# Optimization experiments

Hardware: AMD Instinct MI355X
Metric: run time of the kernel (lower is better)

## Reference

```python
import jax, jax.numpy as jnp
import numpy as np

FS = 4096.0
TRAIN_KERNEL = 4
TRAIN_STRIDE = 0.25
BATCH = 1024
NPERSEG = 4096          # fftlength * fs
NOVERLAP = NPERSEG // 2 # default overlap
FL, FH = 20.0, 500.0


def _welch(data):
    """Faithful port of _torch_welch with average='mean' (which is a SUM over segments
    in the original code), off by the same constant factor as the original."""
    N, nsample = data.shape
    nstride = NPERSEG - NOVERLAP
    nseg = int(np.ceil((nsample - NPERSEG) / nstride)) + 1
    # frame indices [nseg, nperseg] (static numpy -> cheap gather)
    idx = np.arange(nseg)[:, None] * nstride + np.arange(NPERSEG)[None, :]
    frames = data[:, idx]                                   # [N, nseg, nperseg]
    n = np.arange(NPERSEG)
    window = (0.5 - 0.5 * np.cos(2.0 * np.pi * n / NPERSEG)).astype(np.float32) * 2.0  # periodic hann * 2
    fd = jnp.fft.rfft(frames * window, axis=-1)             # [N, nseg, nfreq]
    power = jnp.real(fd) ** 2 + jnp.imag(fd) ** 2
    psd = jnp.sum(power, axis=1)                            # original 'mean' branch uses sum
    T = nsample * FS
    return psd / T                                          # [N, nfreq]


def setup_inputs() -> dict:
    key = jax.random.key(0)
    k1, k2 = jax.random.split(key)
    T = int(TRAIN_KERNEL * FS)  # 16384
    pred = jax.random.normal(k1, (BATCH, T), dtype=jnp.float32)
    target = jax.random.normal(k2, (BATCH, T), dtype=jnp.float32)
    return {"pred": pred, "target": target}


def reference(pred, target):
    res = target - pred
    s = int(TRAIN_STRIDE * FS)                     # 1024 samples per stride
    shape_x = int(TRAIN_KERNEL / TRAIN_STRIDE)     # 16
    # cross[i] = res[:, i*s:(i+1)*s].flatten() -> reshape/transpose, no loop
    def to_cross(x):
        return x[:, : shape_x * s].reshape(BATCH, shape_x, s).transpose(1, 0, 2).reshape(shape_x, BATCH * s)
    cross_res = to_cross(res)
    cross_target = to_cross(target)

    psd_res = _welch(cross_res)                    # [shape_x, nfreq]
    psd_target = _welch(cross_target)

    nfreq = NPERSEG // 2 + 1
    freq = np.linspace(0.0, FS / 2.0, nfreq)
    mask = jnp.asarray((FL < freq) & (freq < FH))
    dfreq = float(freq[1] - freq[0])
    scale = FH - FL

    psd_res = jnp.where(mask, psd_res, 0.0)
    psd_ratio = psd_res / psd_target
    loss = jnp.sum(psd_ratio, axis=1) * dfreq / scale  # [shape_x]
    return jnp.mean(loss[-8:]) * loss.shape[0]
```

## Files before the change

### kernel.cpp

```cpp
#include <hip/hip_runtime.h>

#define NSEG 511
#define NROWS 8
#define ROW0 8
#define K0 21
#define KEND 500
#define NFREQ 479
#define ACC_STRIDE 512
#define ACC_ELEMS (2 * NROWS * ACC_STRIDE)
#define NREP 8
#define NBLOCKS (2 * NROWS * NSEG)

__device__ __forceinline__ int sw(int i) { return i ^ (((i >> 5) & 7) << 2); }

__device__ __forceinline__ int dr_pos(int k) {
    return ((k >> 9) & 3) + 4 * ((k >> 6) & 7) + 32 * ((k >> 3) & 7) + 256 * (k & 7);
}

__device__ __forceinline__ float2 cmul(float2 a, float2 b) {
    return make_float2(fmaf(a.x, b.x, -a.y * b.y), fmaf(a.x, b.y, a.y * b.x));
}
__device__ __forceinline__ float2 cadd(float2 a, float2 b) { return make_float2(a.x + b.x, a.y + b.y); }
__device__ __forceinline__ float2 csub(float2 a, float2 b) { return make_float2(a.x - b.x, a.y - b.y); }

__device__ __forceinline__ void dft8(float2& x0, float2& x1, float2& x2, float2& x3,
                                     float2& x4, float2& x5, float2& x6, float2& x7) {
    const float C45 = 0.70710678118654752440f;
    float2 t0 = cadd(x0, x4), u0 = csub(x0, x4);
    float2 t1 = cadd(x1, x5), u1 = csub(x1, x5);
    float2 t2 = cadd(x2, x6), u2 = csub(x2, x6);
    float2 t3 = cadd(x3, x7), u3 = csub(x3, x7);
    float2 s0 = cadd(t0, t2), d0 = csub(t0, t2);
    float2 s1 = cadd(t1, t3), d1 = csub(t1, t3);
    float2 v1 = make_float2(C45 * (u1.x + u1.y), C45 * (u1.y - u1.x));
    float2 v2 = make_float2(u2.y, -u2.x);
    float2 v3 = make_float2(C45 * (u3.y - u3.x), -C45 * (u3.x + u3.y));
    float2 s2 = cadd(u0, v2), d2 = csub(u0, v2);
    float2 s3 = cadd(v1, v3), d3 = csub(v1, v3);
    float2 mid1 = make_float2(d1.y, -d1.x);
    float2 mid3 = make_float2(d3.y, -d3.x);
    x0 = cadd(s0, s1); x4 = csub(s0, s1);
    x2 = cadd(d0, mid1); x6 = csub(d0, mid1);
    x1 = cadd(s2, s3); x5 = csub(s2, s3);
    x3 = cadd(d2, mid3); x7 = csub(d2, mid3);
}

__device__ __forceinline__ void twiddle8cs(float2& x1, float2& x2, float2& x3, float2& x4,
                                           float2& x5, float2& x6, float2& x7,
                                           float c, float s) {
    float2 w1 = make_float2(c, s);
    float2 w2 = cmul(w1, w1);
    float2 w3 = cmul(w2, w1);
    float2 w4 = cmul(w2, w2);
    float2 w5 = cmul(w4, w1);
    float2 w6 = cmul(w3, w3);
    float2 w7 = cmul(w4, w3);
    x1 = cmul(x1, w1); x2 = cmul(x2, w2); x3 = cmul(x3, w3);
    x4 = cmul(x4, w4); x5 = cmul(x5, w5); x6 = cmul(x6, w6);
    x7 = cmul(x7, w7);
}

__global__ __launch_bounds__(256)
void psd_kernel(const float* __restrict__ pred,
                const float* __restrict__ target,
                float* __restrict__ acc) {
    __shared__ float2 buf[2048];

    const int bid = blockIdx.x;
    const int seg = bid % NSEG;
    const int row = (bid / NSEG) % NROWS + ROW0;
    const int sig = bid / (NSEG * NROWS);
    const int tid = threadIdx.x;
    float* accR = acc + (bid & (NREP - 1)) * ACC_ELEMS;

    const float2* t2p = (const float2*)target;
    const float2* p2p = (const float2*)pred;

    const float WA = 3.06796157577128245e-3f;
    const float CD = 0.99999882344642529f;
    const float SD = 1.53398018628476550e-3f;
    const float H  = 0.70710678118654752440f;
    float sa, ca;
    __sincosf((float)tid * WA, &sa, &ca);

    const int base2 = 2 * seg * 8192 + row * 512 + tid;
    float2 x0, x1, x2, x3, x4, x5, x6, x7;
#define LOADW(R, X, CE, SE)                                                  \
    {                                                                        \
        int idx2 = base2 + ((R) >> 1) * 8192 + ((R) & 1) * 256;              \
        float2 v = t2p[idx2];                                                \
        if (sig == 0) { float2 p = p2p[idx2]; v.x -= p.x; v.y -= p.y; }      \
        float cr = (CE), sr = (SE);                                          \
        X = make_float2(v.x * (1.0f - cr),                                   \
                        v.y * (1.0f - (cr * CD - sr * SD)));                 \
    }
    LOADW(0, x0, ca, sa)
    LOADW(1, x1, H * (ca - sa), H * (sa + ca))
    LOADW(2, x2, -sa, ca)
    LOADW(3, x3, -H * (ca + sa), H * (ca - sa))
    LOADW(4, x4, -ca, -sa)
    LOADW(5, x5, H * (sa - ca), -H * (sa + ca))
    LOADW(6, x6, sa, -ca)
    LOADW(7, x7, H * (ca + sa), H * (sa - ca))
#undef LOADW

    dft8(x0, x1, x2, x3, x4, x5, x6, x7);
    twiddle8cs(x1, x2, x3, x4, x5, x6, x7, ca, -sa);
    buf[sw(tid)]        = x0;
    buf[sw(tid + 256)]  = x1;
    buf[sw(tid + 512)]  = x2;
    buf[sw(tid + 768)]  = x3;
    buf[sw(tid + 1024)] = x4;
    buf[sw(tid + 1280)] = x5;
    buf[sw(tid + 1536)] = x6;
    buf[sw(tid + 1792)] = x7;
    __syncthreads();

    {
        const int pb = tid >> 5, q0 = tid & 31;
        const int baseB = q0 + 256 * pb;
        x0 = buf[sw(baseB)];
        x1 = buf[sw(baseB + 32)];
        x2 = buf[sw(baseB + 64)];
        x3 = buf[sw(baseB + 96)];
        x4 = buf[sw(baseB + 128)];
        x5 = buf[sw(baseB + 160)];
        x6 = buf[sw(baseB + 192)];
        x7 = buf[sw(baseB + 224)];
        dft8(x0, x1, x2, x3, x4, x5, x6, x7);
        float sb, cb;
        __sincosf((float)q0 * -2.45436926061702596e-2f, &sb, &cb);
        twiddle8cs(x1, x2, x3, x4, x5, x6, x7, cb, sb);
        buf[sw(baseB)]       = x0;
        buf[sw(baseB + 32)]  = x1;
        buf[sw(baseB + 64)]  = x2;
        buf[sw(baseB + 96)]  = x3;
        buf[sw(baseB + 128)] = x4;
        buf[sw(baseB + 160)] = x5;
        buf[sw(baseB + 192)] = x6;
        buf[sw(baseB + 224)] = x7;
    }
    __syncthreads();

    {
        const int pb2 = tid >> 5, j2 = (tid >> 2) & 7, mq = tid & 3;
        const int baseC = mq + 32 * j2 + 256 * pb2;
        x0 = buf[sw(baseC)];
        x1 = buf[sw(baseC + 4)];
        x2 = buf[sw(baseC + 8)];
        x3 = buf[sw(baseC + 12)];
        x4 = buf[sw(baseC + 16)];
        x5 = buf[sw(baseC + 20)];
        x6 = buf[sw(baseC + 24)];
        x7 = buf[sw(baseC + 28)];
        dft8(x0, x1, x2, x3, x4, x5, x6, x7);
        const float TC1 = 0.98078528040323044913f, TS1 = -0.19509032201612826785f;
        const float TC2 = 0.92387953251128675613f, TS2 = -0.38268343236508977173f;
        const float TC3 = 0.83146961230254523708f, TS3 = -0.55557023301960222474f;
        float cc = (mq & 2) ? ((mq & 1) ? TC3 : TC2) : ((mq & 1) ? TC1 : 1.0f);
        float ss = (mq & 2) ? ((mq & 1) ? TS3 : TS2) : ((mq & 1) ? TS1 : 0.0f);
        twiddle8cs(x1, x2, x3, x4, x5, x6, x7, cc, ss);
        buf[sw(baseC)]      = x0;
        buf[sw(baseC + 4)]  = x1;
        buf[sw(baseC + 8)]  = x2;
        buf[sw(baseC + 12)] = x3;
        buf[sw(baseC + 16)] = x4;
        buf[sw(baseC + 20)] = x5;
        buf[sw(baseC + 24)] = x6;
        buf[sw(baseC + 28)] = x7;
    }
    __syncthreads();

    float4* b4 = (float4*)buf;
#define STAGE_D(G)                                                           \
    {                                                                        \
        int pbase = sw(4 * (tid + 256 * (G)));                               \
        float4 lo = b4[(pbase >> 1)];                                        \
        float4 hi = b4[(pbase >> 1) + 1];                                    \
        float2 a0 = make_float2(lo.x, lo.y), a1 = make_float2(lo.z, lo.w);   \
        float2 a2 = make_float2(hi.x, hi.y), a3 = make_float2(hi.z, hi.w);   \
        float2 S0 = cadd(a0, a2), D0 = csub(a0, a2);                         \
        float2 S1 = cadd(a1, a3), D1 = csub(a1, a3);                         \
        float2 mi = make_float2(D1.y, -D1.x);                                \
        float2 X0 = cadd(S0, S1), X2 = csub(S0, S1);                         \
        float2 X1 = cadd(D0, mi), X3 = csub(D0, mi);                         \
        b4[(pbase >> 1)]     = make_float4(X0.x, X0.y, X1.x, X1.y);          \
        b4[(pbase >> 1) + 1] = make_float4(X2.x, X2.y, X3.x, X3.y);          \
    }
    STAGE_D(0) STAGE_D(1)
#undef STAGE_D
    __syncthreads();

    {
        int k = K0 + tid;
        float sn0, cs0;
        __sincosf(-1.53398078788564123e-3f * (float)k, &sn0, &cs0);
#define UNTANGLE(KK, CS, SN)                                                 \
        {                                                                    \
            int kk = (KK);                                                   \
            if (kk < KEND) {                                                 \
                float2 zk = buf[sw(dr_pos(kk))];                             \
                float2 zn = buf[sw(dr_pos(2048 - kk))];                      \
                float Ex = 0.5f * (zk.x + zn.x);                             \
                float Ey = 0.5f * (zk.y - zn.y);                             \
                float Ox = 0.5f * (zk.y + zn.y);                             \
                float Oy = -0.5f * (zk.x - zn.x);                            \
                float xr = Ex + Ox * (CS) - Oy * (SN);                       \
                float xi = Ey + Ox * (SN) + Oy * (CS);                       \
                float pw = xr * xr + xi * xi;                                \
                atomicAdd(&accR[(sig * NROWS + (row - ROW0)) * ACC_STRIDE + (kk - K0)], pw); \
            }                                                                \
        }
        UNTANGLE(k, cs0, sn0)
        {
            const float CU = 0.98078528040323044913f;
            const float SU = 0.19509032201612826785f;
            float cs1 = cs0 * CU + sn0 * SU;
            float sn1 = sn0 * CU - cs0 * SU;
            UNTANGLE(k + 256, cs1, sn1)
        }
#undef UNTANGLE
    }
}

__global__ __launch_bounds__(256)
void reduce_kernel(const float* __restrict__ acc, float* __restrict__ out) {
    __shared__ float sh[256];
    int tid = threadIdx.x;
    float sum = 0.0f;
    for (int n = tid; n < NROWS * NFREQ; n += 256) {
        int r = n / NFREQ, k = n % NFREQ;
        float num = 0.0f, den = 0.0f;
        #pragma unroll
        for (int rep = 0; rep < NREP; ++rep) {
            num += acc[rep * ACC_ELEMS + r * ACC_STRIDE + k];
            den += acc[rep * ACC_ELEMS + (NROWS + r) * ACC_STRIDE + k];
        }
        sum += num / den;
    }
    sh[tid] = sum;
    __syncthreads();
    for (int s = 128; s > 0; s >>= 1) {
        if (tid < s) sh[tid] += sh[tid + s];
        __syncthreads();
    }
    if (tid == 0) out[0] = sh[0] * (1.0f / 240.0f);
}

extern "C" void kernel_launch(void* const* d_in, const int* in_sizes, int n_in,
                              void* d_out, int out_size, void* d_ws, size_t ws_size,
                              hipStream_t stream) {
    const float* pred = (const float*)d_in[0];
    const float* target = (const float*)d_in[1];
    float* acc = (float*)d_ws;

    hipMemsetAsync(acc, 0, NREP * ACC_ELEMS * sizeof(float), stream);
    psd_kernel<<<NBLOCKS, 256, 0, stream>>>(pred, target, acc);
    reduce_kernel<<<1, 256, 0, stream>>>(acc, (float*)d_out);
}
```

Measured before the change: 188.6 us.

## Process four overlapping segments per block, reusing half the loaded frame

Each block now handles four consecutive Welch segments instead of one. It reuses the overlapping half of the raw input between segments and prefetches the next half before the FFT stages. Window weights and twiddles are computed once per block. Power is accumulated in registers with one atomic per frequency per block instead of per segment. The last radix-4 stage now writes only the two needed outputs into a separate natural-order buffer. This cuts block count, global loads and atomics, but serialises segments within a block and adds shared memory that may reduce occupancy.

```diff
diff --git a/kernel.cpp b/kernel.cpp
--- a/kernel.cpp
+++ b/kernel.cpp
@@ -9,13 +9,12 @@
 #define ACC_STRIDE 512
 #define ACC_ELEMS (2 * NROWS * ACC_STRIDE)
 #define NREP 8
-#define NBLOCKS (2 * NROWS * NSEG)
+#define SPB 4
+#define NGROUPS 128
+#define NBLOCKS (2 * NROWS * NGROUPS)
 
 __device__ __forceinline__ int sw(int i) { return i ^ (((i >> 5) & 7) << 2); }
-
-__device__ __forceinline__ int dr_pos(int k) {
-    return ((k >> 9) & 3) + 4 * ((k >> 6) & 7) + 32 * ((k >> 3) & 7) + 256 * (k & 7);
-}
+__device__ __forceinline__ int ms(int m) { return m ^ ((m >> 6) & 7); }
 
 __device__ __forceinline__ float2 cmul(float2 a, float2 b) {
     return make_float2(fmaf(a.x, b.x, -a.y * b.y), fmaf(a.x, b.y, a.y * b.x));
@@ -65,16 +64,37 @@
                 const float* __restrict__ target,
                 float* __restrict__ acc) {
     __shared__ float2 buf[2048];
+    __shared__ float2 nat[1024];
 
     const int bid = blockIdx.x;
-    const int seg = bid % NSEG;
-    const int row = (bid / NSEG) % NROWS + ROW0;
-    const int sig = bid / (NSEG * NROWS);
+    const int grp = bid % NGROUPS;
+    const int row = (bid / NGROUPS) % NROWS + ROW0;
+    const int sig = bid / (NGROUPS * NROWS);
     const int tid = threadIdx.x;
+    const int seg0 = grp * SPB;
+    const int ns = (seg0 + SPB <= NSEG) ? SPB : (NSEG - seg0);
     float* accR = acc + (bid & (NREP - 1)) * ACC_ELEMS;
 
     const float2* t2p = (const float2*)target;
     const float2* p2p = (const float2*)pred;
+
+    const int base = 2 * seg0 * 8192 + row * 512 + tid;
+#define LOADRAW(X, IDX)                                                      \
+    {                                                                        \
+        int _i = (IDX);                                                      \
+        float2 v = t2p[_i];                                                  \
+        if (sig == 0) { float2 p = p2p[_i]; v.x -= p.x; v.y -= p.y; }        \
+        X = v;                                                               \
+    }
+    float2 r0, r1, r2, r3, r4, r5, r6, r7;
+    LOADRAW(r0, base)
+    LOADRAW(r1, base + 256)
+    LOADRAW(r2, base + 8192)
+    LOADRAW(r3, base + 8448)
+    LOADRAW(r4, base + 16384)
+    LOADRAW(r5, base + 16640)
+    LOADRAW(r6, base + 24576)
+    LOADRAW(r7, base + 24832)
 
     const float WA = 3.06796157577128245e-3f;
     const float CD = 0.99999882344642529f;
@@ -82,145 +102,172 @@
     const float H  = 0.70710678118654752440f;
     float sa, ca;
     __sincosf((float)tid * WA, &sa, &ca);
-
-    const int base2 = 2 * seg * 8192 + row * 512 + tid;
-    float2 x0, x1, x2, x3, x4, x5, x6, x7;
-#define LOADW(R, X, CE, SE)                                                  \
-    {                                                                        \
-        int idx2 = base2 + ((R) >> 1) * 8192 + ((R) & 1) * 256;              \
-        float2 v = t2p[idx2];                                                \
-        if (sig == 0) { float2 p = p2p[idx2]; v.x -= p.x; v.y -= p.y; }      \
-        float cr = (CE), sr = (SE);                                          \
-        X = make_float2(v.x * (1.0f - cr),                                   \
-                        v.y * (1.0f - (cr * CD - sr * SD)));                 \
-    }
-    LOADW(0, x0, ca, sa)
-    LOADW(1, x1, H * (ca - sa), H * (sa + ca))
-    LOADW(2, x2, -sa, ca)
-    LOADW(3, x3, -H * (ca + sa), H * (ca - sa))
-    LOADW(4, x4, -ca, -sa)
-    LOADW(5, x5, H * (sa - ca), -H * (sa + ca))
-    LOADW(6, x6, sa, -ca)
-    LOADW(7, x7, H * (ca + sa), H * (sa - ca))
-#undef LOADW
-
-    dft8(x0, x1, x2, x3, x4, x5, x6, x7);
-    twiddle8cs(x1, x2, x3, x4, x5, x6, x7, ca, -sa);
-    buf[sw(tid)]        = x0;
-    buf[sw(tid + 256)]  = x1;
-    buf[sw(tid + 512)]  = x2;
-    buf[sw(tid + 768)]  = x3;
-    buf[sw(tid + 1024)] = x4;
-    buf[sw(tid + 1280)] = x5;
-    buf[sw(tid + 1536)] = x6;
-    buf[sw(tid + 1792)] = x7;
-    __syncthreads();
-
+    float2 wv0, wv1, wv2, wv3, wv4, wv5, wv6, wv7;
+#define MKW(W, CE, SE) { float cr = (CE), sr = (SE);                         \
+        W = make_float2(1.0f - cr, 1.0f - (cr * CD - sr * SD)); }
+    MKW(wv0, ca, sa)
+    MKW(wv1, H * (ca - sa), H * (sa + ca))
+    MKW(wv2, -sa, ca)
+    MKW(wv3, -H * (ca + sa), H * (ca - sa))
+    MKW(wv4, -ca, -sa)
+    MKW(wv5, H * (sa - ca), -H * (sa + ca))
+    MKW(wv6, sa, -ca)
+    MKW(wv7, H * (ca + sa), H * (sa - ca))
+#undef MKW
+    float sb, cb;
+    __sincosf((float)(tid & 31) * -2.45436926061702596e-2f, &sb, &cb);
+    float cc, ss;
     {
-        const int pb = tid >> 5, q0 = tid & 31;
-        const int baseB = q0 + 256 * pb;
-        x0 = buf[sw(baseB)];
-        x1 = buf[sw(baseB + 32)];
-        x2 = buf[sw(baseB + 64)];
-        x3 = buf[sw(baseB + 96)];
-        x4 = buf[sw(baseB + 128)];
-        x5 = buf[sw(baseB + 160)];
-        x6 = buf[sw(baseB + 192)];
-        x7 = buf[sw(baseB + 224)];
-        dft8(x0, x1, x2, x3, x4, x5, x6, x7);
-        float sb, cb;
-        __sincosf((float)q0 * -2.45436926061702596e-2f, &sb, &cb);
-        twiddle8cs(x1, x2, x3, x4, x5, x6, x7, cb, sb);
-        buf[sw(baseB)]       = x0;
-        buf[sw(baseB + 32)]  = x1;
-        buf[sw(baseB + 64)]  = x2;
-        buf[sw(baseB + 96)]  = x3;
-        buf[sw(baseB + 128)] = x4;
-        buf[sw(baseB + 160)] = x5;
-        buf[sw(baseB + 192)] = x6;
-        buf[sw(baseB + 224)] = x7;
-    }
-    __syncthreads();
-
-    {
-        const int pb2 = tid >> 5, j2 = (tid >> 2) & 7, mq = tid & 3;
-        const int baseC = mq + 32 * j2 + 256 * pb2;
-        x0 = buf[sw(baseC)];
-        x1 = buf[sw(baseC + 4)];
-        x2 = buf[sw(baseC + 8)];
-        x3 = buf[sw(baseC + 12)];
-        x4 = buf[sw(baseC + 16)];
-        x5 = buf[sw(baseC + 20)];
-        x6 = buf[sw(baseC + 24)];
-        x7 = buf[sw(baseC + 28)];
-        dft8(x0, x1, x2, x3, x4, x5, x6, x7);
         const float TC1 = 0.98078528040323044913f, TS1 = -0.19509032201612826785f;
         const float TC2 = 0.92387953251128675613f, TS2 = -0.38268343236508977173f;
         const float TC3 = 0.83146961230254523708f, TS3 = -0.55557023301960222474f;
-        float cc = (mq & 2) ? ((mq & 1) ? TC3 : TC2) : ((mq & 1) ? TC1 : 1.0f);
-        float ss = (mq & 2) ? ((mq & 1) ? TS3 : TS2) : ((mq & 1) ? TS1 : 0.0f);
-        twiddle8cs(x1, x2, x3, x4, x5, x6, x7, cc, ss);
-        buf[sw(baseC)]      = x0;
-        buf[sw(baseC + 4)]  = x1;
-        buf[sw(baseC + 8)]  = x2;
-        buf[sw(baseC + 12)] = x3;
-        buf[sw(baseC + 16)] = x4;
-        buf[sw(baseC + 20)] = x5;
-        buf[sw(baseC + 24)] = x6;
-        buf[sw(baseC + 28)] = x7;
-    }
-    __syncthreads();
-
+        int mq = tid & 3;
+        cc = (mq & 2) ? ((mq & 1) ? TC3 : TC2) : ((mq & 1) ? TC1 : 1.0f);
+        ss = (mq & 2) ? ((mq & 1) ? TS3 : TS2) : ((mq & 1) ? TS1 : 0.0f);
+    }
+    float sn0, cs0, sn1, cs1;
+    __sincosf(-1.53398078788564123e-3f * (float)(K0 + tid), &sn0, &cs0);
+    {
+        const float CU = 0.98078528040323044913f;
+        const float SU = 0.19509032201612826785f;
+        cs1 = cs0 * CU + sn0 * SU;
+        sn1 = sn0 * CU - cs0 * SU;
+    }
+
+    float pw1 = 0.0f, pw2 = 0.0f;
     float4* b4 = (float4*)buf;
-#define STAGE_D(G)                                                           \
-    {                                                                        \
-        int pbase = sw(4 * (tid + 256 * (G)));                               \
-        float4 lo = b4[(pbase >> 1)];                                        \
-        float4 hi = b4[(pbase >> 1) + 1];                                    \
-        float2 a0 = make_float2(lo.x, lo.y), a1 = make_float2(lo.z, lo.w);   \
-        float2 a2 = make_float2(hi.x, hi.y), a3 = make_float2(hi.z, hi.w);   \
-        float2 S0 = cadd(a0, a2), D0 = csub(a0, a2);                         \
-        float2 S1 = cadd(a1, a3), D1 = csub(a1, a3);                         \
-        float2 mi = make_float2(D1.y, -D1.x);                                \
-        float2 X0 = cadd(S0, S1), X2 = csub(S0, S1);                         \
-        float2 X1 = cadd(D0, mi), X3 = csub(D0, mi);                         \
-        b4[(pbase >> 1)]     = make_float4(X0.x, X0.y, X1.x, X1.y);          \
-        b4[(pbase >> 1) + 1] = make_float4(X2.x, X2.y, X3.x, X3.y);          \
-    }
-    STAGE_D(0) STAGE_D(1)
-#undef STAGE_D
-    __syncthreads();
+
+    #pragma unroll 1
+    for (int s = 0; s < ns; ++s) {
+        float2 x0 = make_float2(r0.x * wv0.x, r0.y * wv0.y);
+        float2 x1 = make_float2(r1.x * wv1.x, r1.y * wv1.y);
+        float2 x2 = make_float2(r2.x * wv2.x, r2.y * wv2.y);
+        float2 x3 = make_float2(r3.x * wv3.x, r3.y * wv3.y);
+        float2 x4 = make_float2(r4.x * wv4.x, r4.y * wv4.y);
+        float2 x5 = make_float2(r5.x * wv5.x, r5.y * wv5.y);
+        float2 x6 = make_float2(r6.x * wv6.x, r6.y * wv6.y);
+        float2 x7 = make_float2(r7.x * wv7.x, r7.y * wv7.y);
+
+        if (s + 1 < ns) {
+            r0 = r4; r1 = r5; r2 = r6; r3 = r7;
+            int nb = base + (s + 1) * 16384;
+            LOADRAW(r4, nb + 16384)
+            LOADRAW(r5, nb + 16640)
+            LOADRAW(r6, nb + 24576)
+            LOADRAW(r7, nb + 24832)
+        }
+
+        dft8(x0, x1, x2, x3, x4, x5, x6, x7);
+        twiddle8cs(x1, x2, x3, x4, x5, x6, x7, ca, -sa);
+        buf[sw(tid)]        = x0;
+        buf[sw(tid + 256)]  = x1;
+        buf[sw(tid + 512)]  = x2;
+        buf[sw(tid + 768)]  = x3;
+        buf[sw(tid + 1024)] = x4;
+        buf[sw(tid + 1280)] = x5;
+        buf[sw(tid + 1536)] = x6;
+        buf[sw(tid + 1792)] = x7;
+        __syncthreads();
+
+        {
+            const int baseB = (tid & 31) + 256 * (tid >> 5);
+            x0 = buf[sw(baseB)];
+            x1 = buf[sw(baseB + 32)];
+            x2 = buf[sw(baseB + 64)];
+            x3 = buf[sw(baseB + 96)];
+            x4 = buf[sw(baseB + 128)];
+            x5 = buf[sw(baseB + 160)];
+            x6 = buf[sw(baseB + 192)];
+            x7 = buf[sw(baseB + 224)];
+            dft8(x0, x1, x2, x3, x4, x5, x6, x7);
+            twiddle8cs(x1, x2, x3, x4, x5, x6, x7, cb, sb);
+            buf[sw(baseB)]       = x0;
+            buf[sw(baseB + 32)]  = x1;
+            buf[sw(baseB + 64)]  = x2;
+            buf[sw(baseB + 96)]  = x3;
+            buf[sw(baseB + 128)] = x4;
+            buf[sw(baseB + 160)] = x5;
+            buf[sw(baseB + 192)] = x6;
+            buf[sw(baseB + 224)] = x7;
+        }
+        __syncthreads();
+
+        {
+            const int baseC = (tid & 3) + 32 * ((tid >> 2) & 7) + 256 * (tid >> 5);
+            x0 = buf[sw(baseC)];
+            x1 = buf[sw(baseC + 4)];
+            x2 = buf[sw(baseC + 8)];
+            x3 = buf[sw(baseC + 12)];
+            x4 = buf[sw(baseC + 16)];
+            x5 = buf[sw(baseC + 20)];
+            x6 = buf[sw(baseC + 24)];
+            x7 = buf[sw(baseC + 28)];
+            dft8(x0, x1, x2, x3, x4, x5, x6, x7);
+            twiddle8cs(x1, x2, x3, x4, x5, x6, x7, cc, ss);
+            buf[sw(baseC)]      = x0;
+            buf[sw(baseC + 4)]  = x1;
+            buf[sw(baseC + 8)]  = x2;
+            buf[sw(baseC + 12)] = x3;
+            buf[sw(baseC + 16)] = x4;
+            buf[sw(baseC + 20)] = x5;
+            buf[sw(baseC + 24)] = x6;
+            buf[sw(baseC + 28)] = x7;
+        }
+        __syncthreads();
+
+#define QUAD(N)                                                              \
+        {                                                                    \
+            int n = (N);                                                     \
+            int q4 = sw(4 * n) >> 1;                                         \
+            float4 lo = b4[q4], hi = b4[q4 + 1];                             \
+            float2 X0 = make_float2((lo.x + hi.x) + (lo.z + hi.z),           \
+                                    (lo.y + hi.y) + (lo.w + hi.w));          \
+            float D0x = lo.x - hi.x, D0y = lo.y - hi.y;                      \
+            float D1x = lo.z - hi.z, D1y = lo.w - hi.w;                      \
+            float2 X3 = make_float2(D0x - D1y, D0y + D1x);                   \
+            int m = 64 * (n & 7) + 8 * ((n >> 3) & 7) + (n >> 6);            \
+            int a = ms(m);                                                   \
+            nat[a] = X0;                                                     \
+            nat[512 + a] = X3;                                               \
+        }
+        QUAD(tid)
+        QUAD(tid + 256)
+#undef QUAD
+        __syncthreads();
+
+        {
+            int k = K0 + tid;
+            float2 zk = nat[ms(k)];
+            float2 zn = nat[512 + ms(512 - k)];
+            float Ex = 0.5f * (zk.x + zn.x);
+            float Ey = 0.5f * (zk.y - zn.y);
+            float Ox = 0.5f * (zk.y + zn.y);
+            float Oy = -0.5f * (zk.x - zn.x);
+            float xr = Ex + Ox * cs0 - Oy * sn0;
+            float xi = Ey + Ox * sn0 + Oy * cs0;
+            pw1 += xr * xr + xi * xi;
+        }
+        if (tid < KEND - K0 - 256) {
+            int k = K0 + 256 + tid;
+            float2 zk = nat[ms(k)];
+            float2 zn = nat[512 + ms(512 - k)];
+            float Ex = 0.5f * (zk.x + zn.x);
+            float Ey = 0.5f * (zk.y - zn.y);
+            float Ox = 0.5f * (zk.y + zn.y);
+            float Oy = -0.5f * (zk.x - zn.x);
+            float xr = Ex + Ox * cs1 - Oy * sn1;
+            float xi = Ey + Ox * sn1 + Oy * cs1;
+            pw2 += xr * xr + xi * xi;
+        }
+        __syncthreads();
+    }
 
     {
-        int k = K0 + tid;
-        float sn0, cs0;
-        __sincosf(-1.53398078788564123e-3f * (float)k, &sn0, &cs0);
-#define UNTANGLE(KK, CS, SN)                                                 \
-        {                                                                    \
-            int kk = (KK);                                                   \
-            if (kk < KEND) {                                                 \
-                float2 zk = buf[sw(dr_pos(kk))];                             \
-                float2 zn = buf[sw(dr_pos(2048 - kk))];                      \
-                float Ex = 0.5f * (zk.x + zn.x);                             \
-                float Ey = 0.5f * (zk.y - zn.y);                             \
-                float Ox = 0.5f * (zk.y + zn.y);                             \
-                float Oy = -0.5f * (zk.x - zn.x);                            \
-                float xr = Ex + Ox * (CS) - Oy * (SN);                       \
-                float xi = Ey + Ox * (SN) + Oy * (CS);                       \
-                float pw = xr * xr + xi * xi;                                \
-                atomicAdd(&accR[(sig * NROWS + (row - ROW0)) * ACC_STRIDE + (kk - K0)], pw); \
-            }                                                                \
-        }
-        UNTANGLE(k, cs0, sn0)
-        {
-            const float CU = 0.98078528040323044913f;
-            const float SU = 0.19509032201612826785f;
-            float cs1 = cs0 * CU + sn0 * SU;
-            float sn1 = sn0 * CU - cs0 * SU;
-            UNTANGLE(k + 256, cs1, sn1)
-        }
-#undef UNTANGLE
-    }
+        int i0 = (sig * NROWS + (row - ROW0)) * ACC_STRIDE;
+        atomicAdd(&accR[i0 + tid], pw1);
+        if (tid < KEND - K0 - 256) atomicAdd(&accR[i0 + 256 + tid], pw2);
+    }
+#undef LOADRAW
 }
 
 __global__ __launch_bounds__(256)
```

Result: faster. 168.8 us (-10.5%).
